# Optimization experiments

Measured on AMD Instinct MI355X. Metric: run time of the kernel, lower is better.

Reference implementation:

```python
import jax, jax.numpy as jnp
import numpy as np

L, H, N = 8192, 1024, 1024
MAX_PHASE = 6.283


def setup_inputs() -> dict:
    key = jax.random.key(0)
    ks = jax.random.split(key, 9)
    input_real = jax.random.uniform(ks[0], (L, H), dtype=jnp.float32)
    input_imag = jax.random.uniform(ks[1], (L, H), dtype=jnp.float32)
    # LRU parameter init (r_min=0, r_max=1, max_phase=6.283)
    u1 = jax.random.uniform(ks[2], (N,), dtype=jnp.float32)
    u2 = jax.random.uniform(ks[3], (N,), dtype=jnp.float32)
    nu_log = jnp.log(-0.5 * jnp.log(u1))
    theta_log = jnp.log(u2 * MAX_PHASE)
    B_real = jax.random.normal(ks[4], (N, H), dtype=jnp.float32) / np.float32(np.sqrt(2 * H))
    B_imag = jax.random.normal(ks[5], (N, H), dtype=jnp.float32) / np.float32(np.sqrt(2 * H))
    C_real = jax.random.normal(ks[6], (H, N), dtype=jnp.float32) / np.float32(np.sqrt(N))
    C_imag = jax.random.normal(ks[7], (H, N), dtype=jnp.float32) / np.float32(np.sqrt(N))
    D = jax.random.normal(ks[8], (H,), dtype=jnp.float32)
    diag_lambda = jnp.exp(jax.lax.complex(-jnp.exp(nu_log), jnp.exp(theta_log)))
    gamma_log = jnp.log(jnp.sqrt(1.0 - jnp.abs(diag_lambda) ** 2))
    return dict(input_real=input_real, input_imag=input_imag,
                nu_log=nu_log, theta_log=theta_log,
                B_real=B_real, B_imag=B_imag,
                C_real=C_real, C_imag=C_imag,
                D=D, gamma_log=gamma_log)


def _binop(e_i, e_j):
    a_i, bu_i = e_i
    a_j, bu_j = e_j
    return a_j * a_i, a_j * bu_i + bu_j


def _lru_forward(input_real, input_imag, nu_log, theta_log,
                 B_real, B_imag, C_real, C_imag, D, gamma_log):
    u = jax.lax.complex(input_real, input_imag)                      # (L, H) complex
    Lambda = jnp.exp(jax.lax.complex(-jnp.exp(nu_log), jnp.exp(theta_log)))  # (N,)
    # Faithful to source: exp(i * gamma_log), NOT exp(gamma_log)
    exp_gamma = jnp.exp(jax.lax.complex(jnp.zeros_like(gamma_log), gamma_log))  # (N,)
    B_norm = jax.lax.complex(B_real, B_imag) * exp_gamma[:, None]    # (N, H)
    Bu = jnp.einsum('lh,nh->ln', u, B_norm)                          # (L, N)
    Lambda_el = jnp.broadcast_to(Lambda[None, :], Bu.shape)          # (L, N)
    _, x = jax.lax.associative_scan(_binop, (Lambda_el, Bu))         # (L, N) states
    C = jax.lax.complex(C_real, C_imag)                              # (H, N)
    Dc = D.astype(C.dtype)                                           # (H,) complex
    y = jnp.real(jnp.einsum('ln,hn->lh', x, C)) + jnp.real(Dc[None, :] * u)
    return y                                                         # (L, H) float32


def reference(input_real, input_imag, nu_log, theta_log,
              B_real, B_imag, C_real, C_imag, D, gamma_log):
    return _lru_forward(input_real, input_imag, nu_log, theta_log,
                        B_real, B_imag, C_real, C_imag, D, gamma_log)
```

## Files before the change

kernel.cpp:

```cpp
#include <hip/hip_runtime.h>
#include <math.h>

#define L_SEQ 8192
#define H_DIM 1024
#define N_DIM 1024
#define K2    2048
#define NCHUNK 64
#define CHUNK 128

typedef unsigned short u16;
typedef __attribute__((ext_vector_type(8))) __bf16 bf16x8;
typedef __attribute__((ext_vector_type(4))) float  f32x4;

__device__ __forceinline__ u16 f2bf(float x) {
    unsigned int u = __float_as_uint(x);
    u = (u + 0x7fffu + ((u >> 16) & 1u)) >> 16;
    return (u16)u;
}
__device__ __forceinline__ float bf2f(u16 h) {
    return __uint_as_float(((unsigned int)h) << 16);
}

__device__ __forceinline__ void gload_lds16(const void* g, void* s) {
    __builtin_amdgcn_global_load_lds(
        (const __attribute__((address_space(1))) unsigned int*)g,
        (__attribute__((address_space(3))) unsigned int*)s, 16, 0, 0);
}

__global__ void pack_u(const float* __restrict__ R, const float* __restrict__ I,
                       u16* __restrict__ A) {
    size_t t = (size_t)blockIdx.x * 256 + threadIdx.x;
    size_t base = t * 4;
    int lrow = (int)(base >> 10);
    int h    = (int)(base & 1023);
    float4 r  = *reinterpret_cast<const float4*>(R + base);
    float4 im = *reinterpret_cast<const float4*>(I + base);
    u16* p0 = A + ((size_t)lrow << 11) + h;
    *reinterpret_cast<ushort4*>(p0) =
        make_ushort4(f2bf(r.x), f2bf(r.y), f2bf(r.z), f2bf(r.w));
    *reinterpret_cast<ushort4*>(p0 + 1024) =
        make_ushort4(f2bf(im.x), f2bf(im.y), f2bf(im.z), f2bf(im.w));
}

__global__ void bnorm_pack(const float* __restrict__ Br, const float* __restrict__ Bi,
                           const float* __restrict__ G, u16* __restrict__ Bp) {
    size_t t = (size_t)blockIdx.x * 256 + threadIdx.x;
    size_t base = t * 4;
    int n = (int)(base >> 10);
    int h = (int)(base & 1023);
    float g = G[n];
    float sg, cg;
    sincosf(g, &sg, &cg);
    float4 br = *reinterpret_cast<const float4*>(Br + base);
    float4 bi = *reinterpret_cast<const float4*>(Bi + base);
    float nr0 = br.x * cg - bi.x * sg, ni0 = br.x * sg + bi.x * cg;
    float nr1 = br.y * cg - bi.y * sg, ni1 = br.y * sg + bi.y * cg;
    float nr2 = br.z * cg - bi.z * sg, ni2 = br.z * sg + bi.z * cg;
    float nr3 = br.w * cg - bi.w * sg, ni3 = br.w * sg + bi.w * cg;
    u16* row0 = Bp + (size_t)n * K2;
    u16* row1 = Bp + (size_t)(N_DIM + n) * K2;
    *reinterpret_cast<ushort4*>(row0 + h) =
        make_ushort4(f2bf(nr0), f2bf(nr1), f2bf(nr2), f2bf(nr3));
    *reinterpret_cast<ushort4*>(row0 + 1024 + h) =
        make_ushort4(f2bf(-ni0), f2bf(-ni1), f2bf(-ni2), f2bf(-ni3));
    *reinterpret_cast<ushort4*>(row1 + h) =
        make_ushort4(f2bf(ni0), f2bf(ni1), f2bf(ni2), f2bf(ni3));
    *reinterpret_cast<ushort4*>(row1 + 1024 + h) =
        make_ushort4(f2bf(nr0), f2bf(nr1), f2bf(nr2), f2bf(nr3));
}

__global__ void pack_C(const float* __restrict__ Cr, const float* __restrict__ Ci,
                       u16* __restrict__ Cp) {
    size_t t = (size_t)blockIdx.x * 256 + threadIdx.x;
    size_t base = t * 4;
    int h = (int)(base >> 10);
    int n = (int)(base & 1023);
    float4 cr = *reinterpret_cast<const float4*>(Cr + base);
    float4 ci = *reinterpret_cast<const float4*>(Ci + base);
    u16* row = Cp + (size_t)h * K2;
    *reinterpret_cast<ushort4*>(row + n) =
        make_ushort4(f2bf(cr.x), f2bf(cr.y), f2bf(cr.z), f2bf(cr.w));
    *reinterpret_cast<ushort4*>(row + 1024 + n) =
        make_ushort4(f2bf(-ci.x), f2bf(-ci.y), f2bf(-ci.z), f2bf(-ci.w));
}

__global__ __launch_bounds__(512, 2) void gemm_pipe(
    const u16* __restrict__ A, const u16* __restrict__ B, int Klen, int lda,
    u16* __restrict__ OutB, int ldo) {
    constexpr int BM     = 256;
    constexpr int ABYTES = BM * 128;
    constexpr int SLOT   = (BM + 256) * 128;
    __shared__ __attribute__((aligned(128))) char lds[2 * SLOT];
    const int tid = threadIdx.x;
    const int l   = tid & 63;
    const int w   = tid >> 6;
    const int wm  = w >> 2;
    const int wn  = w & 3;
    const long bm = (long)blockIdx.x * BM;
    const long bn = (long)blockIdx.y * 256;

    f32x4 acc[8][4];
#pragma unroll
    for (int i = 0; i < 8; ++i)
#pragma unroll
        for (int j = 0; j < 4; ++j) acc[i][j] = (f32x4){0.f, 0.f, 0.f, 0.f};

    const int    swzcol    = (((tid & 7) ^ ((tid >> 3) & 7)) << 4);
    const size_t rowstride = (size_t)lda * 2;
    const size_t a_src0    = (size_t)(bm + (tid >> 3)) * rowstride + swzcol;
    const size_t b_src0    = (size_t)(bn + (tid >> 3)) * rowstride + swzcol;
    const char*  Agb       = (const char*)A;
    const char*  Bgb       = (const char*)B;

    auto STAGE = [&](int kt, int sl) {
        const size_t kofs = (size_t)kt * 128;
        char* la = lds + sl * SLOT + tid * 16;
        char* lb = lds + sl * SLOT + ABYTES + tid * 16;
#pragma unroll
        for (int j = 0; j < 4; ++j)
            gload_lds16(Agb + a_src0 + (size_t)j * 64 * rowstride + kofs,
                        la + j * 8192);
#pragma unroll
        for (int j = 0; j < 4; ++j)
            gload_lds16(Bgb + b_src0 + (size_t)j * 64 * rowstride + kofs,
                        lb + j * 8192);
    };

    const int l15   = l & 15;
    const int lslot = l >> 4;

    const int nt = Klen / 64;
    STAGE(0, 0);
    STAGE(1, 1);

    for (int t = 0; t < nt; ++t) {
        const int s = t & 1;
        if (t < nt - 1) asm volatile("s_waitcnt vmcnt(8)" ::: "memory");
        else            asm volatile("s_waitcnt vmcnt(0)" ::: "memory");
        __builtin_amdgcn_sched_barrier(0);
        __builtin_amdgcn_s_barrier();
        __builtin_amdgcn_sched_barrier(0);

        const char* lA = lds + s * SLOT;
        const char* lB = lA + ABYTES;
#pragma unroll
        for (int kk = 0; kk < 2; ++kk) {
            bf16x8 af[8], bg[4];
#pragma unroll
            for (int mi = 0; mi < 8; ++mi) {
                int r   = wm * 128 + mi * 16 + l15;
                int sl3 = ((kk << 2) | lslot) ^ (r & 7);
                af[mi]  = *reinterpret_cast<const bf16x8*>(lA + r * 128 + sl3 * 16);
            }
#pragma unroll
            for (int ni = 0; ni < 4; ++ni) {
                int r   = wn * 64 + ni * 16 + l15;
                int sl3 = ((kk << 2) | lslot) ^ (r & 7);
                bg[ni]  = *reinterpret_cast<const bf16x8*>(lB + r * 128 + sl3 * 16);
            }
            __builtin_amdgcn_s_setprio(1);
#pragma unroll
            for (int mi = 0; mi < 8; ++mi)
#pragma unroll
                for (int ni = 0; ni < 4; ++ni)
                    acc[mi][ni] = __builtin_amdgcn_mfma_f32_16x16x32_bf16(
                        af[mi], bg[ni], acc[mi][ni], 0, 0, 0);
            __builtin_amdgcn_s_setprio(0);
        }
        __builtin_amdgcn_sched_barrier(0);
        __builtin_amdgcn_s_barrier();
        __builtin_amdgcn_sched_barrier(0);
        if (t + 2 < nt) STAGE(t + 2, s);
    }

#pragma unroll
    for (int mi = 0; mi < 8; ++mi) {
        const long row0 = bm + wm * 128 + mi * 16 + ((l >> 4) << 2);
#pragma unroll
        for (int ni = 0; ni < 4; ++ni) {
            const long col = bn + wn * 64 + ni * 16 + l15;
#pragma unroll
            for (int r = 0; r < 4; ++r)
                OutB[(size_t)(row0 + r) * ldo + col] = f2bf(acc[mi][ni][r]);
        }
    }
}

__global__ __launch_bounds__(256, 2) void gemm_small(
    const u16* __restrict__ A, const u16* __restrict__ B, int Klen, int lda,
    float* __restrict__ OutF, int ldo,
    const float* __restrict__ Dv, const float* __restrict__ Ur) {
    constexpr int ABYTES = 128 * 128;
    constexpr int SLOT   = 2 * ABYTES;
    __shared__ __attribute__((aligned(128))) char lds[2 * SLOT];
    const int tid = threadIdx.x;
    const int l   = tid & 63;
    const int w   = tid >> 6;
    const int wm  = w >> 1;
    const int wn  = w & 1;
    const long bm = (long)blockIdx.x * 128;
    const long bn = (long)blockIdx.y * 128;

    f32x4 acc[4][4];
#pragma unroll
    for (int i = 0; i < 4; ++i)
#pragma unroll
        for (int j = 0; j < 4; ++j) acc[i][j] = (f32x4){0.f, 0.f, 0.f, 0.f};

    const int    lr        = tid >> 3;
    const int    swzcol    = (((tid & 7) ^ (lr & 7)) << 4);
    const size_t rowstride = (size_t)lda * 2;
    const size_t a_src0    = (size_t)(bm + lr) * rowstride + swzcol;
    const size_t b_src0    = (size_t)(bn + lr) * rowstride + swzcol;
    const char*  Agb       = (const char*)A;
    const char*  Bgb       = (const char*)B;

    auto STAGE = [&](int kt, int sl) {
        const size_t kofs = (size_t)kt * 128;
        char* la = lds + sl * SLOT + tid * 16;
        char* lb = lds + sl * SLOT + ABYTES + tid * 16;
#pragma unroll
        for (int j = 0; j < 4; ++j)
            gload_lds16(Agb + a_src0 + (size_t)j * 32 * rowstride + kofs,
                        la + j * 4096);
#pragma unroll
        for (int j = 0; j < 4; ++j)
            gload_lds16(Bgb + b_src0 + (size_t)j * 32 * rowstride + kofs,
                        lb + j * 4096);
    };

    const int l15   = l & 15;
    const int lslot = l >> 4;

    const int nt = Klen / 64;
    STAGE(0, 0);
    STAGE(1, 1);

    for (int t = 0; t < nt; ++t) {
        const int s = t & 1;
        if (t < nt - 1) asm volatile("s_waitcnt vmcnt(8)" ::: "memory");
        else            asm volatile("s_waitcnt vmcnt(0)" ::: "memory");
        __builtin_amdgcn_sched_barrier(0);
        __builtin_amdgcn_s_barrier();
        __builtin_amdgcn_sched_barrier(0);

        const char* lA = lds + s * SLOT;
        const char* lB = lA + ABYTES;
#pragma unroll
        for (int kk = 0; kk < 2; ++kk) {
            bf16x8 af[4], bg[4];
#pragma unroll
            for (int mi = 0; mi < 4; ++mi) {
                int r   = wm * 64 + mi * 16 + l15;
                int sl3 = ((kk << 2) | lslot) ^ (r & 7);
                af[mi]  = *reinterpret_cast<const bf16x8*>(lA + r * 128 + sl3 * 16);
            }
#pragma unroll
            for (int ni = 0; ni < 4; ++ni) {
                int r   = wn * 64 + ni * 16 + l15;
                int sl3 = ((kk << 2) | lslot) ^ (r & 7);
                bg[ni]  = *reinterpret_cast<const bf16x8*>(lB + r * 128 + sl3 * 16);
            }
            __builtin_amdgcn_s_setprio(1);
#pragma unroll
            for (int mi = 0; mi < 4; ++mi)
#pragma unroll
                for (int ni = 0; ni < 4; ++ni)
                    acc[mi][ni] = __builtin_amdgcn_mfma_f32_16x16x32_bf16(
                        af[mi], bg[ni], acc[mi][ni], 0, 0, 0);
            __builtin_amdgcn_s_setprio(0);
        }
        __builtin_amdgcn_sched_barrier(0);
        __builtin_amdgcn_s_barrier();
        __builtin_amdgcn_sched_barrier(0);
        if (t + 2 < nt) STAGE(t + 2, s);
    }

#pragma unroll
    for (int mi = 0; mi < 4; ++mi) {
        const long row0 = bm + wm * 64 + mi * 16 + ((l >> 4) << 2);
#pragma unroll
        for (int ni = 0; ni < 4; ++ni) {
            const long col = bn + wn * 64 + ni * 16 + l15;
            const float d = Dv[col];
#pragma unroll
            for (int r = 0; r < 4; ++r) {
                size_t o = (size_t)(row0 + r) * ldo + col;
                OutF[o] = acc[mi][ni][r] + d * Ur[o];
            }
        }
    }
}

__global__ void scan_sum(const u16* __restrict__ X,
                         const float* __restrict__ nu_log,
                         const float* __restrict__ theta_log,
                         float* __restrict__ Acr, float* __restrict__ Aci,
                         float* __restrict__ bcr, float* __restrict__ bci) {
    int n = blockIdx.y * 256 + threadIdx.x;
    int c = blockIdx.x;
    float mag = expf(-expf(nu_log[n]));
    float th  = expf(theta_log[n]);
    float sg, cg;
    sincosf(th, &sg, &cg);
    float lr = mag * cg, li = mag * sg;
    float sr = 0.f, si = 0.f, pr = 1.f, pi = 0.f;
    size_t base = (size_t)c * CHUNK * K2 + n;
    for (int j = 0; j < CHUNK; ++j) {
        size_t idx = base + (size_t)j * K2;
        float br = bf2f(X[idx]), bi = bf2f(X[idx + 1024]);
        float nr = lr * sr - li * si + br;
        float ni = lr * si + li * sr + bi;
        sr = nr; si = ni;
        float qr = lr * pr - li * pi;
        float qi = lr * pi + li * pr;
        pr = qr; pi = qi;
    }
    Acr[c * N_DIM + n] = pr; Aci[c * N_DIM + n] = pi;
    bcr[c * N_DIM + n] = sr; bci[c * N_DIM + n] = si;
}

__global__ void scan_carry(const float* __restrict__ Acr, const float* __restrict__ Aci,
                           const float* __restrict__ bcr, const float* __restrict__ bci,
                           float* __restrict__ car, float* __restrict__ cai) {
    int n = blockIdx.x * 256 + threadIdx.x;
    float sr = 0.f, si = 0.f;
    for (int c = 0; c < NCHUNK; ++c) {
        car[c * N_DIM + n] = sr; cai[c * N_DIM + n] = si;
        float ar = Acr[c * N_DIM + n], ai = Aci[c * N_DIM + n];
        float nr = ar * sr - ai * si + bcr[c * N_DIM + n];
        float ni = ar * si + ai * sr + bci[c * N_DIM + n];
        sr = nr; si = ni;
    }
}

__global__ void scan_apply(u16* __restrict__ X,
                           const float* __restrict__ nu_log,
                           const float* __restrict__ theta_log,
                           const float* __restrict__ car, const float* __restrict__ cai) {
    int n = blockIdx.y * 256 + threadIdx.x;
    int c = blockIdx.x;
    float mag = expf(-expf(nu_log[n]));
    float th  = expf(theta_log[n]);
    float sg, cg;
    sincosf(th, &sg, &cg);
    float lr = mag * cg, li = mag * sg;
    float sr = car[c * N_DIM + n], si = cai[c * N_DIM + n];
    size_t base = (size_t)c * CHUNK * K2 + n;
    for (int j = 0; j < CHUNK; ++j) {
        size_t idx = base + (size_t)j * K2;
        float br = bf2f(X[idx]), bi = bf2f(X[idx + 1024]);
        float nr = lr * sr - li * si + br;
        float ni = lr * si + li * sr + bi;
        sr = nr; si = ni;
        X[idx] = f2bf(sr); X[idx + 1024] = f2bf(si);
    }
}

extern "C" void kernel_launch(void* const* d_in, const int* in_sizes, int n_in,
                              void* d_out, int out_size, void* d_ws, size_t ws_size,
                              hipStream_t stream) {
    (void)in_sizes; (void)n_in; (void)out_size; (void)ws_size;
    const float* input_real = (const float*)d_in[0];
    const float* input_imag = (const float*)d_in[1];
    const float* nu_log     = (const float*)d_in[2];
    const float* theta_log  = (const float*)d_in[3];
    const float* B_real     = (const float*)d_in[4];
    const float* B_imag     = (const float*)d_in[5];
    const float* C_real     = (const float*)d_in[6];
    const float* C_imag     = (const float*)d_in[7];
    const float* D          = (const float*)d_in[8];
    const float* gamma_log  = (const float*)d_in[9];
    float* y = (float*)d_out;

    char* ws = (char*)d_ws;
    float* Acr = (float*)(ws + (8 << 10));
    float* Aci = Acr + NCHUNK * N_DIM;
    float* bcr = Aci + NCHUNK * N_DIM;
    float* bci = bcr + NCHUNK * N_DIM;
    float* car = bci + NCHUNK * N_DIM;
    float* cai = car + NCHUNK * N_DIM;
    u16* Ap   = (u16*)(ws + ((size_t)2 << 20));
    u16* Cp   = Ap;
    u16* Bp   = (u16*)(ws + ((size_t)34 << 20));
    u16* X    = (u16*)(ws + ((size_t)42 << 20));

    pack_u<<<(L_SEQ * H_DIM / 4) / 256, 256, 0, stream>>>(input_real, input_imag, Ap);
    bnorm_pack<<<(N_DIM * H_DIM / 4) / 256, 256, 0, stream>>>(B_real, B_imag, gamma_log, Bp);
    gemm_pipe<<<dim3(L_SEQ / 256, K2 / 256), 512, 0, stream>>>(
        Ap, Bp, K2, K2, X, K2);
    scan_sum<<<dim3(NCHUNK, N_DIM / 256), 256, 0, stream>>>(
        X, nu_log, theta_log, Acr, Aci, bcr, bci);
    scan_carry<<<N_DIM / 256, 256, 0, stream>>>(Acr, Aci, bcr, bci, car, cai);
    scan_apply<<<dim3(NCHUNK, N_DIM / 256), 256, 0, stream>>>(
        X, nu_log, theta_log, car, cai);
    pack_C<<<(H_DIM * N_DIM / 4) / 256, 256, 0, stream>>>(C_real, C_imag, Cp);
    gemm_small<<<dim3(L_SEQ / 128, H_DIM / 128), 256, 0, stream>>>(
        X, Cp, K2, K2, y, H_DIM, D, input_real);
}
```

Before: 171.8 us.

## Interleave GEMM half-tile prefetch with MFMA and vectorize chunked scan with smaller chunks

The main GEMM now stages A and B in half-tiles and issues those loads between split MFMA groups, so global-to-LDS transfers overlap with compute. The aim is to hide load latency that used to sit behind whole-tile barriers. The scan kernels now process two channels per thread with 32-bit packed bf16 loads and stores. Chunks shrink from 128 to 32 rows, giving four times as many chunks, which adds parallelism to the sequential scans at the cost of a longer carry pass. The carry buffers are moved to reuse the workspace region that held Bp, which is only safe if Bp is no longer needed by then.

```diff
diff --git a/kernel.cpp b/kernel.cpp
--- a/kernel.cpp
+++ b/kernel.cpp
@@ -5,8 +5,8 @@
 #define H_DIM 1024
 #define N_DIM 1024
 #define K2    2048
-#define NCHUNK 64
-#define CHUNK 128
+#define NCHUNK 256
+#define CHUNK 32
 
 typedef unsigned short u16;
 typedef __attribute__((ext_vector_type(8))) __bf16 bf16x8;
@@ -87,16 +87,15 @@
 __global__ __launch_bounds__(512, 2) void gemm_pipe(
     const u16* __restrict__ A, const u16* __restrict__ B, int Klen, int lda,
     u16* __restrict__ OutB, int ldo) {
-    constexpr int BM     = 256;
-    constexpr int ABYTES = BM * 128;
-    constexpr int SLOT   = (BM + 256) * 128;
+    constexpr int ABYTES = 256 * 128;
+    constexpr int SLOT   = 2 * ABYTES;
     __shared__ __attribute__((aligned(128))) char lds[2 * SLOT];
     const int tid = threadIdx.x;
     const int l   = tid & 63;
     const int w   = tid >> 6;
     const int wm  = w >> 2;
     const int wn  = w & 3;
-    const long bm = (long)blockIdx.x * BM;
+    const long bm = (long)blockIdx.x * 256;
     const long bn = (long)blockIdx.y * 256;
 
     f32x4 acc[8][4];
@@ -105,73 +104,101 @@
 #pragma unroll
         for (int j = 0; j < 4; ++j) acc[i][j] = (f32x4){0.f, 0.f, 0.f, 0.f};
 
-    const int    swzcol    = (((tid & 7) ^ ((tid >> 3) & 7)) << 4);
+    const int    lr        = tid >> 3;
+    const int    swzcol    = (((tid & 7) ^ (lr & 7)) << 4);
     const size_t rowstride = (size_t)lda * 2;
-    const size_t a_src0    = (size_t)(bm + (tid >> 3)) * rowstride + swzcol;
-    const size_t b_src0    = (size_t)(bn + (tid >> 3)) * rowstride + swzcol;
+    const size_t a_src0    = (size_t)(bm + lr) * rowstride + swzcol;
+    const size_t b_src0    = (size_t)(bn + lr) * rowstride + swzcol;
     const char*  Agb       = (const char*)A;
     const char*  Bgb       = (const char*)B;
-
-    auto STAGE = [&](int kt, int sl) {
+    const int nt = Klen / 64;
+
+    auto STAGE_A = [&](int kt, int h) {
+        if (kt >= nt) return;
         const size_t kofs = (size_t)kt * 128;
-        char* la = lds + sl * SLOT + tid * 16;
-        char* lb = lds + sl * SLOT + ABYTES + tid * 16;
-#pragma unroll
-        for (int j = 0; j < 4; ++j)
-            gload_lds16(Agb + a_src0 + (size_t)j * 64 * rowstride + kofs,
-                        la + j * 8192);
-#pragma unroll
-        for (int j = 0; j < 4; ++j)
-            gload_lds16(Bgb + b_src0 + (size_t)j * 64 * rowstride + kofs,
-                        lb + j * 8192);
+        char* d = lds + (kt & 1) * SLOT + h * 16384 + tid * 16;
+#pragma unroll
+        for (int j = 0; j < 2; ++j)
+            gload_lds16(Agb + a_src0 + (size_t)(h * 128 + j * 64) * rowstride + kofs,
+                        d + j * 8192);
+    };
+    auto STAGE_B = [&](int kt, int h) {
+        if (kt >= nt) return;
+        const size_t kofs = (size_t)kt * 128;
+        char* d = lds + (kt & 1) * SLOT + ABYTES + h * 16384 + tid * 16;
+#pragma unroll
+        for (int j = 0; j < 2; ++j)
+            gload_lds16(Bgb + b_src0 + (size_t)(h * 128 + j * 64) * rowstride + kofs,
+                        d + j * 8192);
     };
 
     const int l15   = l & 15;
     const int lslot = l >> 4;
 
-    const int nt = Klen / 64;
-    STAGE(0, 0);
-    STAGE(1, 1);
+    auto READ_A = [&](bf16x8 (&af)[8], const char* lA, int kk) {
+#pragma unroll
+        for (int mi = 0; mi < 8; ++mi) {
+            int r   = wm * 128 + mi * 16 + l15;
+            int sl3 = ((kk << 2) | lslot) ^ (r & 7);
+            af[mi]  = *reinterpret_cast<const bf16x8*>(lA + r * 128 + sl3 * 16);
+        }
+    };
+    auto READ_B = [&](bf16x8 (&bg)[4], const char* lB, int kk) {
+#pragma unroll
+        for (int ni = 0; ni < 4; ++ni) {
+            int r   = wn * 64 + ni * 16 + l15;
+            int sl3 = ((kk << 2) | lslot) ^ (r & 7);
+            bg[ni]  = *reinterpret_cast<const bf16x8*>(lB + r * 128 + sl3 * 16);
+        }
+    };
+    auto MFMA_Q = [&](bf16x8 (&af)[8], bf16x8 (&bg)[4], int qn) {
+        __builtin_amdgcn_s_setprio(1);
+#pragma unroll
+        for (int mi = 0; mi < 8; ++mi)
+#pragma unroll
+            for (int nj = 0; nj < 2; ++nj)
+                acc[mi][qn * 2 + nj] = __builtin_amdgcn_mfma_f32_16x16x32_bf16(
+                    af[mi], bg[qn * 2 + nj], acc[mi][qn * 2 + nj], 0, 0, 0);
+        __builtin_amdgcn_s_setprio(0);
+    };
+
+#define SBAR  do { __builtin_amdgcn_sched_barrier(0);                        \
+    __builtin_amdgcn_s_barrier();                                            \
+    __builtin_amdgcn_sched_barrier(0); } while (0)
+#define LGKM0 do { asm volatile("s_waitcnt lgkmcnt(0)" ::: "memory");        \
+    __builtin_amdgcn_sched_barrier(0); } while (0)
+
+    STAGE_A(0, 0); STAGE_B(0, 0); STAGE_A(0, 1); STAGE_B(0, 1);
+    STAGE_A(1, 0); STAGE_B(1, 0);
+    asm volatile("s_waitcnt vmcnt(4)" ::: "memory");
+    SBAR;
+
+    bf16x8 af0[8], af1[8], bg0[4], bg1[4];
 
     for (int t = 0; t < nt; ++t) {
-        const int s = t & 1;
-        if (t < nt - 1) asm volatile("s_waitcnt vmcnt(8)" ::: "memory");
+        const char* lA = lds + (t & 1) * SLOT;
+        const char* lB = lA + ABYTES;
+        READ_A(af0, lA, 0);
+        READ_B(bg0, lB, 0);
+        STAGE_A(t + 1, 1);
+        LGKM0;
+        MFMA_Q(af0, bg0, 0);
+        READ_A(af1, lA, 1);
+        READ_B(bg1, lB, 1);
+        STAGE_B(t + 1, 1);
+        MFMA_Q(af0, bg0, 1);
+        LGKM0;
+        SBAR;
+        STAGE_A(t + 2, 0);
+        MFMA_Q(af1, bg1, 0);
+        STAGE_B(t + 2, 0);
+        MFMA_Q(af1, bg1, 1);
+        if (t < nt - 2) asm volatile("s_waitcnt vmcnt(4)" ::: "memory");
         else            asm volatile("s_waitcnt vmcnt(0)" ::: "memory");
-        __builtin_amdgcn_sched_barrier(0);
-        __builtin_amdgcn_s_barrier();
-        __builtin_amdgcn_sched_barrier(0);
-
-        const char* lA = lds + s * SLOT;
-        const char* lB = lA + ABYTES;
-#pragma unroll
-        for (int kk = 0; kk < 2; ++kk) {
-            bf16x8 af[8], bg[4];
-#pragma unroll
-            for (int mi = 0; mi < 8; ++mi) {
-                int r   = wm * 128 + mi * 16 + l15;
-                int sl3 = ((kk << 2) | lslot) ^ (r & 7);
-                af[mi]  = *reinterpret_cast<const bf16x8*>(lA + r * 128 + sl3 * 16);
-            }
-#pragma unroll
-            for (int ni = 0; ni < 4; ++ni) {
-                int r   = wn * 64 + ni * 16 + l15;
-                int sl3 = ((kk << 2) | lslot) ^ (r & 7);
-                bg[ni]  = *reinterpret_cast<const bf16x8*>(lB + r * 128 + sl3 * 16);
-            }
-            __builtin_amdgcn_s_setprio(1);
-#pragma unroll
-            for (int mi = 0; mi < 8; ++mi)
-#pragma unroll
-                for (int ni = 0; ni < 4; ++ni)
-                    acc[mi][ni] = __builtin_amdgcn_mfma_f32_16x16x32_bf16(
-                        af[mi], bg[ni], acc[mi][ni], 0, 0, 0);
-            __builtin_amdgcn_s_setprio(0);
-        }
-        __builtin_amdgcn_sched_barrier(0);
-        __builtin_amdgcn_s_barrier();
-        __builtin_amdgcn_sched_barrier(0);
-        if (t + 2 < nt) STAGE(t + 2, s);
-    }
+        SBAR;
+    }
+#undef SBAR
+#undef LGKM0
 
 #pragma unroll
     for (int mi = 0; mi < 8; ++mi) {
@@ -297,27 +324,43 @@
                          const float* __restrict__ theta_log,
                          float* __restrict__ Acr, float* __restrict__ Aci,
                          float* __restrict__ bcr, float* __restrict__ bci) {
-    int n = blockIdx.y * 256 + threadIdx.x;
-    int c = blockIdx.x;
-    float mag = expf(-expf(nu_log[n]));
-    float th  = expf(theta_log[n]);
-    float sg, cg;
-    sincosf(th, &sg, &cg);
-    float lr = mag * cg, li = mag * sg;
-    float sr = 0.f, si = 0.f, pr = 1.f, pi = 0.f;
-    size_t base = (size_t)c * CHUNK * K2 + n;
+    int n0 = (blockIdx.y * 256 + threadIdx.x) * 2;
+    int c  = blockIdx.x;
+    float lr0, li0, lr1, li1;
+    {
+        float m0 = expf(-expf(nu_log[n0]));
+        float t0 = expf(theta_log[n0]);
+        float s0, c0; sincosf(t0, &s0, &c0);
+        lr0 = m0 * c0; li0 = m0 * s0;
+        float m1 = expf(-expf(nu_log[n0 + 1]));
+        float t1 = expf(theta_log[n0 + 1]);
+        float s1, c1; sincosf(t1, &s1, &c1);
+        lr1 = m1 * c1; li1 = m1 * s1;
+    }
+    float sr0 = 0.f, si0 = 0.f, pr0 = 1.f, pi0 = 0.f;
+    float sr1 = 0.f, si1 = 0.f, pr1 = 1.f, pi1 = 0.f;
+    size_t base = (size_t)c * CHUNK * K2 + n0;
     for (int j = 0; j < CHUNK; ++j) {
         size_t idx = base + (size_t)j * K2;
-        float br = bf2f(X[idx]), bi = bf2f(X[idx + 1024]);
-        float nr = lr * sr - li * si + br;
-        float ni = lr * si + li * sr + bi;
-        sr = nr; si = ni;
-        float qr = lr * pr - li * pi;
-        float qi = lr * pi + li * pr;
-        pr = qr; pi = qi;
-    }
-    Acr[c * N_DIM + n] = pr; Aci[c * N_DIM + n] = pi;
-    bcr[c * N_DIM + n] = sr; bci[c * N_DIM + n] = si;
+        unsigned int ru = *reinterpret_cast<const unsigned int*>(X + idx);
+        unsigned int iu = *reinterpret_cast<const unsigned int*>(X + idx + 1024);
+        float br0 = bf2f((u16)ru), br1 = bf2f((u16)(ru >> 16));
+        float bi0 = bf2f((u16)iu), bi1 = bf2f((u16)(iu >> 16));
+        float nr0 = lr0 * sr0 - li0 * si0 + br0;
+        float ni0 = lr0 * si0 + li0 * sr0 + bi0;
+        sr0 = nr0; si0 = ni0;
+        float nr1 = lr1 * sr1 - li1 * si1 + br1;
+        float ni1 = lr1 * si1 + li1 * sr1 + bi1;
+        sr1 = nr1; si1 = ni1;
+        float q0 = lr0 * pr0 - li0 * pi0, q1 = lr0 * pi0 + li0 * pr0;
+        pr0 = q0; pi0 = q1;
+        float q2 = lr1 * pr1 - li1 * pi1, q3 = lr1 * pi1 + li1 * pr1;
+        pr1 = q2; pi1 = q3;
+    }
+    Acr[c * N_DIM + n0] = pr0; Aci[c * N_DIM + n0] = pi0;
+    bcr[c * N_DIM + n0] = sr0; bci[c * N_DIM + n0] = si0;
+    Acr[c * N_DIM + n0 + 1] = pr1; Aci[c * N_DIM + n0 + 1] = pi1;
+    bcr[c * N_DIM + n0 + 1] = sr1; bci[c * N_DIM + n0 + 1] = si1;
 }
 
 __global__ void scan_carry(const float* __restrict__ Acr, const float* __restrict__ Aci,
@@ -338,22 +381,38 @@
                            const float* __restrict__ nu_log,
                            const float* __restrict__ theta_log,
                            const float* __restrict__ car, const float* __restrict__ cai) {
-    int n = blockIdx.y * 256 + threadIdx.x;
-    int c = blockIdx.x;
-    float mag = expf(-expf(nu_log[n]));
-    float th  = expf(theta_log[n]);
-    float sg, cg;
-    sincosf(th, &sg, &cg);
-    float lr = mag * cg, li = mag * sg;
-    float sr = car[c * N_DIM + n], si = cai[c * N_DIM + n];
-    size_t base = (size_t)c * CHUNK * K2 + n;
+    int n0 = (blockIdx.y * 256 + threadIdx.x) * 2;
+    int c  = blockIdx.x;
+    float lr0, li0, lr1, li1;
+    {
+        float m0 = expf(-expf(nu_log[n0]));
+        float t0 = expf(theta_log[n0]);
+        float s0, c0; sincosf(t0, &s0, &c0);
+        lr0 = m0 * c0; li0 = m0 * s0;
+        float m1 = expf(-expf(nu_log[n0 + 1]));
+        float t1 = expf(theta_log[n0 + 1]);
+        float s1, c1; sincosf(t1, &s1, &c1);
+        lr1 = m1 * c1; li1 = m1 * s1;
+    }
+    float sr0 = car[c * N_DIM + n0],     si0 = cai[c * N_DIM + n0];
+    float sr1 = car[c * N_DIM + n0 + 1], si1 = cai[c * N_DIM + n0 + 1];
+    size_t base = (size_t)c * CHUNK * K2 + n0;
     for (int j = 0; j < CHUNK; ++j) {
         size_t idx = base + (size_t)j * K2;
-        float br = bf2f(X[idx]), bi = bf2f(X[idx + 1024]);
-        float nr = lr * sr - li * si + br;
-        float ni = lr * si + li * sr + bi;
-        sr = nr; si = ni;
-        X[idx] = f2bf(sr); X[idx + 1024] = f2bf(si);
+        unsigned int ru = *reinterpret_cast<const unsigned int*>(X + idx);
+        unsigned int iu = *reinterpret_cast<const unsigned int*>(X + idx + 1024);
+        float br0 = bf2f((u16)ru), br1 = bf2f((u16)(ru >> 16));
+        float bi0 = bf2f((u16)iu), bi1 = bf2f((u16)(iu >> 16));
+        float nr0 = lr0 * sr0 - li0 * si0 + br0;
+        float ni0 = lr0 * si0 + li0 * sr0 + bi0;
+        sr0 = nr0; si0 = ni0;
+        float nr1 = lr1 * sr1 - li1 * si1 + br1;
+        float ni1 = lr1 * si1 + li1 * sr1 + bi1;
+        sr1 = nr1; si1 = ni1;
+        *reinterpret_cast<unsigned int*>(X + idx) =
+            (unsigned int)f2bf(sr0) | ((unsigned int)f2bf(sr1) << 16);
+        *reinterpret_cast<unsigned int*>(X + idx + 1024) =
+            (unsigned int)f2bf(si0) | ((unsigned int)f2bf(si1) << 16);
     }
 }
 
@@ -374,25 +433,25 @@
     float* y = (float*)d_out;
 
     char* ws = (char*)d_ws;
-    float* Acr = (float*)(ws + (8 << 10));
+    u16* Ap   = (u16*)(ws + ((size_t)2 << 20));
+    u16* Cp   = Ap;
+    u16* Bp   = (u16*)(ws + ((size_t)34 << 20));
+    float* Acr = (float*)(ws + ((size_t)34 << 20));
     float* Aci = Acr + NCHUNK * N_DIM;
     float* bcr = Aci + NCHUNK * N_DIM;
     float* bci = bcr + NCHUNK * N_DIM;
     float* car = bci + NCHUNK * N_DIM;
     float* cai = car + NCHUNK * N_DIM;
-    u16* Ap   = (u16*)(ws + ((size_t)2 << 20));
-    u16* Cp   = Ap;
-    u16* Bp   = (u16*)(ws + ((size_t)34 << 20));
     u16* X    = (u16*)(ws + ((size_t)42 << 20));
 
     pack_u<<<(L_SEQ * H_DIM / 4) / 256, 256, 0, stream>>>(input_real, input_imag, Ap);
     bnorm_pack<<<(N_DIM * H_DIM / 4) / 256, 256, 0, stream>>>(B_real, B_imag, gamma_log, Bp);
     gemm_pipe<<<dim3(L_SEQ / 256, K2 / 256), 512, 0, stream>>>(
         Ap, Bp, K2, K2, X, K2);
-    scan_sum<<<dim3(NCHUNK, N_DIM / 256), 256, 0, stream>>>(
+    scan_sum<<<dim3(NCHUNK, N_DIM / 512), 256, 0, stream>>>(
         X, nu_log, theta_log, Acr, Aci, bcr, bci);
     scan_carry<<<N_DIM / 256, 256, 0, stream>>>(Acr, Aci, bcr, bci, car, cai);
-    scan_apply<<<dim3(NCHUNK, N_DIM / 256), 256, 0, stream>>>(
+    scan_apply<<<dim3(NCHUNK, N_DIM / 512), 256, 0, stream>>>(
         X, nu_log, theta_log, car, cai);
     pack_C<<<(H_DIM * N_DIM / 4) / 256, 256, 0, stream>>>(C_real, C_imag, Cp);
     gemm_small<<<dim3(L_SEQ / 128, H_DIM / 128), 256, 0, stream>>>(
```

Measured after the change: 170.7 us. About the same (-0.6%).
